# Kernel optimization log

Measured on AMD Instinct MI355X. Metric: run time of the kernel, lower is better.

## Reference

```python
import jax, jax.numpy as jnp
import numpy as np

VOCAB = 32000; PAD = 0
NHID = 512; H = 8; NK = 64; NV = 64; NL = 4
B = 16; S = 511; L = S + 1
N = B * S            # graph nodes after reshape(-1, n_hid)
E = 131072           # edges per graph
EPS = 1e-5
PATTERN = [0, 0, 1, 1, 0, 0, 1, 1]  # n_head==8 -> [gt,gt,attr,attr,gt,gt,attr,attr]


def setup_inputs() -> dict:
    key = jax.random.key(0)
    ks = iter(jax.random.split(key, 48))
    r = lambda *sh: jax.random.normal(next(ks), sh, jnp.float32) * 0.02
    inp = {}
    emb = jax.random.normal(next(ks), (VOCAB, NHID), jnp.float32) * 0.1
    inp['in_embed_w'] = emb.at[PAD].set(0.0)            # padding_idx row is zero
    inp['pos_embed_w'] = jax.random.normal(next(ks), (L, NHID), jnp.float32) * 0.1
    inp['qkv_w'] = r(NL, NHID, H * (2 * NK + NV)); inp['qkv_b'] = r(NL, H * (2 * NK + NV))
    inp['attn_out_w'] = r(NL, H * NV, NHID); inp['attn_out_b'] = r(NL, NHID)
    inp['ff1_w'] = r(NL, NHID, 4 * NHID); inp['ff1_b'] = r(NL, 4 * NHID)
    inp['ff2_w'] = r(NL, 4 * NHID, NHID); inp['ff2_b'] = r(NL, NHID)
    inp['sage1_w'] = r(H, NHID, NHID); inp['sage1_b'] = r(H, NHID)
    inp['sage2_w'] = r(H, NHID, NHID); inp['sage2_b'] = r(H, NHID)
    inp['gc3_w'] = r(H, NHID, NHID // H); inp['gc3_b'] = r(H, NHID // H)
    inp['gcn_ff1_w'] = r(NHID, NHID); inp['gcn_ff1_b'] = r(NHID)
    inp['gcn_ff2_w'] = r(NHID, NHID); inp['gcn_ff2_b'] = r(NHID)
    inp['ln_g'] = jnp.ones((NHID,), jnp.float32)
    inp['ln_b'] = jnp.zeros((NHID,), jnp.float32)
    inp['in_idxs'] = jax.random.randint(next(ks), (B, S), 1, VOCAB)
    inp['mask'] = jnp.ones((B, L, H, L), dtype=bool)
    inp['gt_src'] = jax.random.randint(next(ks), (E,), 0, N)
    inp['gt_dst'] = jax.random.randint(next(ks), (E,), 0, N)
    inp['attr_src'] = jax.random.randint(next(ks), (E,), 0, N)
    inp['attr_dst'] = jax.random.randint(next(ks), (E,), 0, N)
    return inp


def _ln(x, g, b):
    mu = x.mean(-1, keepdims=True)
    v = ((x - mu) ** 2).mean(-1, keepdims=True)
    return (x - mu) / jnp.sqrt(v + EPS) * g + b


def _encode(in_embed_w, pos_embed_w, qkv_w, qkv_b, attn_out_w, attn_out_b,
            ff1_w, ff1_b, ff2_w, ff2_b, sage1_w, sage1_b, sage2_w, sage2_b,
            gc3_w, gc3_b, gcn_ff1_w, gcn_ff1_b, gcn_ff2_w, gcn_ff2_b, ln_g, ln_b,
            in_idxs, mask, gt_src, gt_dst, attr_src, attr_dst):
    # --- embed (pad one pad-token column at the front) ---
    pad_idxs = jnp.pad(in_idxs, ((0, 0), (1, 0)), constant_values=PAD)
    h = in_embed_w[pad_idxs] + pos_embed_w[jnp.arange(L)]        # [B,L,NHID]
    m = mask.transpose(0, 2, 1, 3)                               # [B,H,L,L]
    # --- transformer blocks ---
    for l in range(NL):
        qkv = (h @ qkv_w[l] + qkv_b[l]).reshape(B, L, H, 2 * NK + NV).transpose(0, 2, 1, 3)
        q, k, v = qkv[..., :NK], qkv[..., NK:2 * NK], qkv[..., 2 * NK:]
        sc = jnp.einsum('bhik,bhjk->bhij', q, k) / np.float32(np.sqrt(NK))
        sc = jnp.where(m, sc, -jnp.inf)
        a = jax.nn.softmax(sc, axis=-1)
        o = jnp.einsum('bhij,bhjd->bhid', a, v).transpose(0, 2, 1, 3).reshape(B, L, H * NV)
        attn_ret = h + (o @ attn_out_w[l] + attn_out_b[l])       # attn module returns x + out
        x = h + attn_ret                                         # block adds x again (faithful)
        h = x + (jax.nn.relu(x @ ff1_w[l] + ff1_b[l]) @ ff2_w[l] + ff2_b[l])
    zg, hg = h[:, 0], h[:, 1:]                                   # [B,NHID], [B,S,NHID]
    # --- GCN over flattened nodes ---
    xf = hg.reshape(N, NHID)
    def deg(idx):
        return jax.ops.segment_sum(jnp.ones((E,), jnp.float32), idx, num_segments=N)
    gdata = []
    for src, dst in ((gt_src, gt_dst), (attr_src, attr_dst)):
        gdata.append((src, dst, deg(dst), deg(src)))             # (src, dst, in_deg, out_deg)
    outs = []
    for i in range(H):
        src, dst, ind, outd = gdata[PATTERN[i]]
        def sage(x, W, b):
            # DGL SAGEConv 'gcn': (sum_neigh + self) / (in_deg + 1) then linear
            agg = jax.ops.segment_sum(x[src], dst, num_segments=N)
            return ((agg + x) / (ind + 1.0)[:, None]) @ W + b
        o = sage(xf, sage1_w[i], sage1_b[i])
        o = sage(o, sage2_w[i], sage2_b[i])
        # DGL GraphConv norm='both' (in>out so weight first)
        f = (o @ gc3_w[i]) * (jnp.maximum(outd, 1.0) ** -0.5)[:, None]
        agg = jax.ops.segment_sum(f[src], dst, num_segments=N)
        outs.append(agg * (jnp.maximum(ind, 1.0) ** -0.5)[:, None] + gc3_b[i])
    xc = jnp.concatenate(outs, axis=-1).reshape(B, S, NHID)
    x = hg + _ln(xc, ln_g, ln_b)
    ff = jax.nn.relu(x @ gcn_ff1_w + gcn_ff1_b) @ gcn_ff2_w + gcn_ff2_b
    zbar = x + _ln(ff, ln_g, ln_b)
    return zbar, zg


def reference(in_embed_w, pos_embed_w, qkv_w, qkv_b, attn_out_w, attn_out_b,
              ff1_w, ff1_b, ff2_w, ff2_b, sage1_w, sage1_b, sage2_w, sage2_b,
              gc3_w, gc3_b, gcn_ff1_w, gcn_ff1_b, gcn_ff2_w, gcn_ff2_b, ln_g, ln_b,
              in_idxs, mask, gt_src, gt_dst, attr_src, attr_dst):
    return _encode(in_embed_w, pos_embed_w, qkv_w, qkv_b, attn_out_w, attn_out_b,
                   ff1_w, ff1_b, ff2_w, ff2_b, sage1_w, sage1_b, sage2_w, sage2_b,
                   gc3_w, gc3_b, gcn_ff1_w, gcn_ff1_b, gcn_ff2_w, gcn_ff2_b, ln_g, ln_b,
                   in_idxs, mask, gt_src, gt_dst, attr_src, attr_dst)
```

## Files before the change

### kernel.cpp

```cpp
#include <hip/hip_runtime.h>
#include <hip/hip_bf16.h>

typedef __hip_bfloat16 bf16;
typedef unsigned short u16;
typedef __attribute__((ext_vector_type(8))) short s16x8;
typedef __attribute__((ext_vector_type(4))) float f32x4;

__device__ __forceinline__ float bfb(unsigned short b) {
    union { unsigned u; float f; } v; v.u = ((unsigned)b) << 16; return v.f;
}
__device__ __forceinline__ float ldin(const void* p, size_t i, bool f32) {
    return f32 ? ((const float*)p)[i] : bfb(((const unsigned short*)p)[i]);
}
__device__ __forceinline__ void ld4(const void* p, size_t i, bool f32,
                                    float& x, float& y, float& z, float& w) {
    if (f32) {
        float4 v = *reinterpret_cast<const float4*>((const float*)p + i);
        x = v.x; y = v.y; z = v.z; w = v.w;
    } else {
        ushort4 u = *reinterpret_cast<const ushort4*>((const unsigned short*)p + i);
        x = bfb(u.x); y = bfb(u.y); z = bfb(u.z); w = bfb(u.w);
    }
}
__device__ __forceinline__ u16 f2b(float x) {
    bf16 h = __float2bfloat16(x);
    return *reinterpret_cast<u16*>(&h);
}
__device__ __forceinline__ void split2(float x, u16& h, u16& l) {
    unsigned u = __float_as_uint(x);
    h = (u16)(u >> 16);
    float rem = x - __uint_as_float(u & 0xFFFF0000u);
    l = f2b(rem);
}

constexpr int C_B = 16, C_S = 511, C_L = 512, C_NHID = 512;
constexpr int C_N = C_B * C_S;
constexpr int C_MTOK = C_B * C_L;
constexpr int C_E = 131072;
constexpr int C_QKVD = 1536;

enum : size_t {
    OFF_H     = 0,
    OFF_QKV   = 4194304,
    OFF_O     = 16777216,
    OFF_X     = 20971520,
    OFF_MID   = 25165824,
    OFF_PRE   = 41943040,
    OFF_T8    = OFF_PRE,
    OFF_GCAT0 = OFF_PRE + 262144,
    OFF_GCAT1 = OFF_GCAT0 + 131072,
    OFF_DCAT0 = OFF_GCAT1 + 131072,
    OFF_DCAT1 = OFF_DCAT0 + 256,
    OFF_DEG   = OFF_DCAT1 + 256,
    OFF_FLAG  = OFF_DEG + 32768
};

__global__ void detect_kernel(const unsigned* __restrict__ g, int* __restrict__ flag) {
    *flag = (g[0] == 0x3F800000u) ? 1 : 0;
}

__global__ __launch_bounds__(256) void embed_kernel(
    const void* __restrict__ emb, const void* __restrict__ pos,
    const int* __restrict__ idxs, const int* __restrict__ flag,
    float* __restrict__ h)
{
    const bool f = (*flag) != 0;
    int token = blockIdx.x;
    int tid = threadIdx.x;
    int b = token >> 9, t = token & 511;
    int id = (t == 0) ? 0 : idxs[b * C_S + t - 1];
    size_t eo = (size_t)id * C_NHID, po = (size_t)t * C_NHID, ho = (size_t)token * C_NHID;
    h[ho + tid]       = ldin(emb, eo + tid, f)       + ldin(pos, po + tid, f);
    h[ho + tid + 256] = ldin(emb, eo + tid + 256, f) + ldin(pos, po + tid + 256, f);
}

__global__ __launch_bounds__(256) void wtrans2_kernel(
    const void* __restrict__ Wsrc, size_t srcOff, const int* __restrict__ flag,
    u16* __restrict__ Bh, u16* __restrict__ Bl, int K, int N)
{
    const bool f = (*flag) != 0;
    __shared__ float s[32][33];
    int nb = blockIdx.x << 5, kb = blockIdx.y << 5;
    int c = threadIdx.x & 31, r0 = (threadIdx.x >> 5) << 2;
#pragma unroll
    for (int i = 0; i < 4; ++i)
        s[r0 + i][c] = ldin(Wsrc, srcOff + (size_t)(kb + r0 + i) * N + nb + c, f);
    __syncthreads();
#pragma unroll
    for (int i = 0; i < 4; ++i) {
        u16 h, l;
        split2(s[c][r0 + i], h, l);
        size_t o = (size_t)(nb + r0 + i) * K + kb + c;
        Bh[o] = h; Bl[o] = l;
    }
}

__global__ __launch_bounds__(256, 2) void msgemm_kernel(
    const float* __restrict__ A,
    const u16* __restrict__ Bh, const u16* __restrict__ Bl,
    const void* __restrict__ biasB, size_t bOff,
    const float* __restrict__ biasF,
    const float* __restrict__ res, float resScale,
    const float* __restrict__ rowDeg, int relu,
    const int* __restrict__ flag,
    float* __restrict__ C, int M, int K, int Nc, int ldc)
{
    const bool f32in = (*flag) != 0;
    __shared__ __align__(16) u16 sAh[128][40];
    __shared__ __align__(16) u16 sAl[128][40];
    __shared__ __align__(16) u16 sBh[64][40];
    __shared__ __align__(16) u16 sBl[64][40];
    const int tid = threadIdx.x;
    const int bm = blockIdx.y << 7, bn = blockIdx.x << 6;
    const int lane = tid & 63, lr = lane & 15, lg = lane >> 4;
    const int wave = tid >> 6, wm = wave >> 1, wn = wave & 1;

    f32x4 acc[4][2];
#pragma unroll
    for (int m = 0; m < 4; ++m)
#pragma unroll
        for (int n = 0; n < 2; ++n) {
            f32x4 z = {0.f, 0.f, 0.f, 0.f};
            acc[m][n] = z;
        }

    const int sr = tid >> 1, sk = (tid & 1) << 4;
    const int am = bm + sr;
    const bool aok = am < M;
    const float* ap = A + (size_t)am * K + sk;
    const int brn = tid >> 2, bk = (tid & 3) << 3;
    const u16* bph = Bh + (size_t)(bn + brn) * K + bk;
    const u16* bpl = Bl + (size_t)(bn + brn) * K + bk;

    for (int k0 = 0; k0 < K; k0 += 32) {
        u16 tah[16], tal[16];
        if (aok) {
#pragma unroll
            for (int i = 0; i < 16; i += 4) {
                float4 v = *reinterpret_cast<const float4*>(ap + k0 + i);
                split2(v.x, tah[i],     tal[i]);
                split2(v.y, tah[i + 1], tal[i + 1]);
                split2(v.z, tah[i + 2], tal[i + 2]);
                split2(v.w, tah[i + 3], tal[i + 3]);
            }
        } else {
#pragma unroll
            for (int i = 0; i < 16; ++i) { tah[i] = 0; tal[i] = 0; }
        }
        s16x8 bh0 = *reinterpret_cast<const s16x8*>(bph + k0);
        s16x8 bl0 = *reinterpret_cast<const s16x8*>(bpl + k0);

        *reinterpret_cast<s16x8*>(&sAh[sr][sk])     = *reinterpret_cast<s16x8*>(&tah[0]);
        *reinterpret_cast<s16x8*>(&sAh[sr][sk + 8]) = *reinterpret_cast<s16x8*>(&tah[8]);
        *reinterpret_cast<s16x8*>(&sAl[sr][sk])     = *reinterpret_cast<s16x8*>(&tal[0]);
        *reinterpret_cast<s16x8*>(&sAl[sr][sk + 8]) = *reinterpret_cast<s16x8*>(&tal[8]);
        *reinterpret_cast<s16x8*>(&sBh[brn][bk]) = bh0;
        *reinterpret_cast<s16x8*>(&sBl[brn][bk]) = bl0;
        __syncthreads();

        s16x8 fah[4], fal[4], fbh[2], fbl[2];
#pragma unroll
        for (int m = 0; m < 4; ++m) {
            fah[m] = *reinterpret_cast<const s16x8*>(&sAh[wm * 64 + m * 16 + lr][lg * 8]);
            fal[m] = *reinterpret_cast<const s16x8*>(&sAl[wm * 64 + m * 16 + lr][lg * 8]);
        }
#pragma unroll
        for (int n = 0; n < 2; ++n) {
            fbh[n] = *reinterpret_cast<const s16x8*>(&sBh[wn * 32 + n * 16 + lr][lg * 8]);
            fbl[n] = *reinterpret_cast<const s16x8*>(&sBl[wn * 32 + n * 16 + lr][lg * 8]);
        }
#pragma unroll
        for (int m = 0; m < 4; ++m)
#pragma unroll
            for (int n = 0; n < 2; ++n) {
                acc[m][n] = __builtin_amdgcn_mfma_f32_16x16x32_bf16(fah[m], fbh[n], acc[m][n], 0, 0, 0);
                acc[m][n] = __builtin_amdgcn_mfma_f32_16x16x32_bf16(fah[m], fbl[n], acc[m][n], 0, 0, 0);
                acc[m][n] = __builtin_amdgcn_mfma_f32_16x16x32_bf16(fal[m], fbh[n], acc[m][n], 0, 0, 0);
            }
        __syncthreads();
    }

#pragma unroll
    for (int m = 0; m < 4; ++m) {
#pragma unroll
        for (int r = 0; r < 4; ++r) {
            int row = bm + wm * 64 + m * 16 + lg * 4 + r;
            if (row >= M) continue;
            float rs = rowDeg ? rsqrtf(fmaxf(rowDeg[row], 1.f)) : 1.f;
#pragma unroll
            for (int n = 0; n < 2; ++n) {
                int col = bn + wn * 32 + n * 16 + lr;
                float v = acc[m][n][r];
                if (biasB) v += ldin(biasB, bOff + col, f32in);
                if (biasF) v += biasF[col];
                v *= rs;
                if (res) v += resScale * res[(size_t)row * Nc + col];
                if (relu) v = fmaxf(v, 0.f);
                C[(size_t)row * ldc + col] = v;
            }
        }
    }
}

__global__ __launch_bounds__(256) void mattn_kernel(
    const float* __restrict__ qkv, float* __restrict__ o_out)
{
    __shared__ __align__(16) u16 sKh[64][72], sKl[64][72];
    __shared__ __align__(16) u16 sVh[64][72], sVl[64][72];
    __shared__ __align__(16) u16 sPh[4][16][72], sPl[4][16][72];
    const int blk = blockIdx.x;
    const int b = blk >> 6, h = (blk >> 3) & 7, qt = blk & 7;
    const int tid = threadIdx.x;
    const int lane = tid & 63, lr = lane & 15, lg = lane >> 4;
    const int w = tid >> 6;

    s16x8 qh[2], ql[2];
    {
        const float* qp = qkv + (size_t)(b * C_L + qt * 64 + w * 16 + lr) * C_QKVD + h * 192;
#pragma unroll
        for (int c = 0; c < 2; ++c) {
            int d0 = c * 32 + lg * 8;
            u16 th[8], tl[8];
#pragma unroll
            for (int i = 0; i < 8; i += 4) {
                float4 v = *reinterpret_cast<const float4*>(qp + d0 + i);
                split2(v.x * 0.125f, th[i],     tl[i]);
                split2(v.y * 0.125f, th[i + 1], tl[i + 1]);
                split2(v.z * 0.125f, th[i + 2], tl[i + 2]);
                split2(v.w * 0.125f, th[i + 3], tl[i + 3]);
            }
            qh[c] = *reinterpret_cast<s16x8*>(th);
            ql[c] = *reinterpret_cast<s16x8*>(tl);
        }
    }

    f32x4 accO[4];
#pragma unroll
    for (int n = 0; n < 4; ++n) { f32x4 z = {0.f, 0.f, 0.f, 0.f}; accO[n] = z; }
    float m[4] = {-3.0e38f, -3.0e38f, -3.0e38f, -3.0e38f};
    float l[4] = {0.f, 0.f, 0.f, 0.f};

    const float* kvb = qkv + (size_t)b * C_L * C_QKVD + h * 192;
    const int kp = tid >> 2;
    const int d0 = (tid & 3) << 4;

    for (int jt = 0; jt < 8; ++jt) {
        __syncthreads();
        {
            const float* kr = kvb + (size_t)(jt * 64 + kp) * C_QKVD + 64 + d0;
            const float* vr = kr + 64;
#pragma unroll
            for (int i = 0; i < 16; i += 4) {
                float4 kv = *reinterpret_cast<const float4*>(kr + i);
                float4 vv = *reinterpret_cast<const float4*>(vr + i);
                u16 th[4], tl[4];
                split2(kv.x, th[0], tl[0]); split2(kv.y, th[1], tl[1]);
                split2(kv.z, th[2], tl[2]); split2(kv.w, th[3], tl[3]);
                *reinterpret_cast<ushort4*>(&sKh[kp][d0 + i]) = *reinterpret_cast<ushort4*>(th);
                *reinterpret_cast<ushort4*>(&sKl[kp][d0 + i]) = *reinterpret_cast<ushort4*>(tl);
                u16 hh, ll;
                split2(vv.x, hh, ll); sVh[d0 + i][kp]     = hh; sVl[d0 + i][kp]     = ll;
                split2(vv.y, hh, ll); sVh[d0 + i + 1][kp] = hh; sVl[d0 + i + 1][kp] = ll;
                split2(vv.z, hh, ll); sVh[d0 + i + 2][kp] = hh; sVl[d0 + i + 2][kp] = ll;
                split2(vv.w, hh, ll); sVh[d0 + i + 3][kp] = hh; sVl[d0 + i + 3][kp] = ll;
            }
        }
        __syncthreads();

        f32x4 accS[4];
#pragma unroll
        for (int n = 0; n < 4; ++n) { f32x4 z = {0.f, 0.f, 0.f, 0.f}; accS[n] = z; }
#pragma unroll
        for (int n = 0; n < 4; ++n)
#pragma unroll
            for (int c = 0; c < 2; ++c) {
                s16x8 kh = *reinterpret_cast<const s16x8*>(&sKh[n * 16 + lr][c * 32 + lg * 8]);
                s16x8 kl = *reinterpret_cast<const s16x8*>(&sKl[n * 16 + lr][c * 32 + lg * 8]);
                accS[n] = __builtin_amdgcn_mfma_f32_16x16x32_bf16(qh[c], kh, accS[n], 0, 0, 0);
                accS[n] = __builtin_amdgcn_mfma_f32_16x16x32_bf16(qh[c], kl, accS[n], 0, 0, 0);
                accS[n] = __builtin_amdgcn_mfma_f32_16x16x32_bf16(ql[c], kh, accS[n], 0, 0, 0);
            }

#pragma unroll
        for (int r = 0; r < 4; ++r) {
            float mt = fmaxf(fmaxf(accS[0][r], accS[1][r]), fmaxf(accS[2][r], accS[3][r]));
            mt = fmaxf(mt, __shfl_xor(mt, 1));
            mt = fmaxf(mt, __shfl_xor(mt, 2));
            mt = fmaxf(mt, __shfl_xor(mt, 4));
            mt = fmaxf(mt, __shfl_xor(mt, 8));
            float mn = fmaxf(m[r], mt);
            float corr = __expf(m[r] - mn);
            m[r] = mn;
            float ps = 0.f;
#pragma unroll
            for (int n = 0; n < 4; ++n) {
                float p = __expf(accS[n][r] - mn);
                accS[n][r] = p;
                ps += p;
            }
            ps += __shfl_xor(ps, 1);
            ps += __shfl_xor(ps, 2);
            ps += __shfl_xor(ps, 4);
            ps += __shfl_xor(ps, 8);
            l[r] = l[r] * corr + ps;
#pragma unroll
            for (int n2 = 0; n2 < 4; ++n2) accO[n2][r] *= corr;
        }

#pragma unroll
        for (int r = 0; r < 4; ++r)
#pragma unroll
            for (int n = 0; n < 4; ++n) {
                u16 hh, ll;
                split2(accS[n][r], hh, ll);
                sPh[w][lg * 4 + r][n * 16 + lr] = hh;
                sPl[w][lg * 4 + r][n * 16 + lr] = ll;
            }
        __syncthreads();

#pragma unroll
        for (int n2 = 0; n2 < 4; ++n2)
#pragma unroll
            for (int c = 0; c < 2; ++c) {
                s16x8 ph = *reinterpret_cast<const s16x8*>(&sPh[w][lr][c * 32 + lg * 8]);
                s16x8 pl = *reinterpret_cast<const s16x8*>(&sPl[w][lr][c * 32 + lg * 8]);
                s16x8 vh = *reinterpret_cast<const s16x8*>(&sVh[n2 * 16 + lr][c * 32 + lg * 8]);
                s16x8 vl = *reinterpret_cast<const s16x8*>(&sVl[n2 * 16 + lr][c * 32 + lg * 8]);
                accO[n2] = __builtin_amdgcn_mfma_f32_16x16x32_bf16(ph, vh, accO[n2], 0, 0, 0);
                accO[n2] = __builtin_amdgcn_mfma_f32_16x16x32_bf16(ph, vl, accO[n2], 0, 0, 0);
                accO[n2] = __builtin_amdgcn_mfma_f32_16x16x32_bf16(pl, vh, accO[n2], 0, 0, 0);
            }
    }

#pragma unroll
    for (int r = 0; r < 4; ++r) {
        float inv = 1.f / l[r];
        float* op = o_out + (size_t)(b * C_L + qt * 64 + w * 16 + lg * 4 + r) * C_NHID + h * 64;
#pragma unroll
        for (int n2 = 0; n2 < 4; ++n2)
            op[n2 * 16 + lr] = accO[n2][r] * inv;
    }
}

__global__ __launch_bounds__(256) void sgemm64b_kernel(
    const void* __restrict__ A, int aIn, size_t aOff, size_t zA,
    const void* __restrict__ Wt, int wIn, size_t wOff, size_t zW,
    const int* __restrict__ flag,
    float* __restrict__ C, size_t zC, int M, int K, int Nc)
{
    const bool f32in = (*flag) != 0;
    const bool aF32 = aIn ? f32in : true;
    const bool wF32 = wIn ? f32in : true;
    const size_t za = aOff + (size_t)blockIdx.z * zA;
    const size_t zw = wOff + (size_t)blockIdx.z * zW;
    float* Cz = C + (size_t)blockIdx.z * zC;

    __shared__ float sA[16][68];
    __shared__ float sB[16][68];
    const int tid = threadIdx.x;
    const int tx = tid & 15, ty = tid >> 4;
    const int bm = blockIdx.y << 6, bn = blockIdx.x << 6;
    float acc[4][4] = {};
    const int la_r = tid >> 2;
    const int la_c = (tid & 3) << 2;
    const int lb_r = tid >> 4;
    const int lb_c = (tid & 15) << 2;

    for (int k0 = 0; k0 < K; k0 += 16) {
        float a0, a1, a2, a3, b0, b1, b2, b3;
        ld4(A, za + (size_t)(bm + la_r) * K + k0 + la_c, aF32, a0, a1, a2, a3);
        ld4(Wt, zw + (size_t)(k0 + lb_r) * Nc + bn + lb_c, wF32, b0, b1, b2, b3);
        sA[la_c + 0][la_r] = a0; sA[la_c + 1][la_r] = a1;
        sA[la_c + 2][la_r] = a2; sA[la_c + 3][la_r] = a3;
        sB[lb_r][lb_c + 0] = b0; sB[lb_r][lb_c + 1] = b1;
        sB[lb_r][lb_c + 2] = b2; sB[lb_r][lb_c + 3] = b3;
        __syncthreads();
#pragma unroll
        for (int kk = 0; kk < 16; ++kk) {
            float av[4], bv[4];
#pragma unroll
            for (int i = 0; i < 4; ++i) av[i] = sA[kk][(ty << 2) + i];
#pragma unroll
            for (int j = 0; j < 4; ++j) bv[j] = sB[kk][(tx << 2) + j];
#pragma unroll
            for (int i = 0; i < 4; ++i)
#pragma unroll
                for (int j = 0; j < 4; ++j)
                    acc[i][j] += av[i] * bv[j];
        }
        __syncthreads();
    }
#pragma unroll
    for (int i = 0; i < 4; ++i)
#pragma unroll
        for (int j = 0; j < 4; ++j)
            Cz[(size_t)(bm + (ty << 2) + i) * Nc + bn + (tx << 2) + j] = acc[i][j];
}

__global__ __launch_bounds__(256) void gcatT2_kernel(
    const float* __restrict__ Gtmp,
    u16* __restrict__ G0h, u16* __restrict__ G0l,
    u16* __restrict__ G1h, u16* __restrict__ G1l)
{
    int idx = blockIdx.x * 256 + threadIdx.x;
    int i = idx >> 15, rem = idx & 32767;
    int k = rem >> 6, c = rem & 63;
    int g = (i >> 1) & 1;
    int slot = (i & 1) + ((i >> 2) << 1);
    u16 h, l;
    split2(Gtmp[idx], h, l);
    size_t o = (size_t)(slot * 64 + c) * 512 + k;
    if (g) { G1h[o] = h; G1l[o] = l; }
    else   { G0h[o] = h; G0l[o] = l; }
}

__global__ __launch_bounds__(256) void xfcopy_kernel(
    const float* __restrict__ h, float* __restrict__ xf)
{
    int idx = blockIdx.x * 256 + threadIdx.x;
    int n = idx >> 9, c = idx & 511;
    int b = n / C_S;
    int s = n - b * C_S;
    xf[idx] = h[(((size_t)(b * C_L + 1 + s)) << 9) + c];
}

__global__ __launch_bounds__(256) void degi_kernel(
    const int* __restrict__ gs, const int* __restrict__ gd,
    const int* __restrict__ as_, const int* __restrict__ ad,
    int* __restrict__ ideg0, int* __restrict__ ideg1,
    float* __restrict__ outd0, float* __restrict__ outd1)
{
    int e = blockIdx.x * 256 + threadIdx.x;
    if (e >= C_E) return;
    atomicAdd(&ideg0[gd[e]], 1);
    atomicAdd(&ideg1[ad[e]], 1);
    atomicAdd(&outd0[gs[e]], 1.f);
    atomicAdd(&outd1[as_[e]], 1.f);
}

__global__ __launch_bounds__(1024) void scan_kernel(
    const int* __restrict__ i0, const int* __restrict__ i1,
    int* __restrict__ r0, int* __restrict__ r1)
{
    __shared__ int part[1024];
    const int t = threadIdx.x;
    const int* d = blockIdx.x ? i1 : i0;
    int* rs = blockIdx.x ? r1 : r0;
    int v[8]; int s = 0;
#pragma unroll
    for (int i = 0; i < 8; ++i) {
        int idx = t * 8 + i;
        v[i] = (idx < C_N) ? d[idx] : 0;
        s += v[i];
    }
    part[t] = s;
    __syncthreads();
    for (int off = 1; off < 1024; off <<= 1) {
        int x = (t >= off) ? part[t - off] : 0;
        __syncthreads();
        part[t] += x;
        __syncthreads();
    }
    int run = part[t] - s;
#pragma unroll
    for (int i = 0; i < 8; ++i) {
        int idx = t * 8 + i;
        if (idx <= C_N) rs[idx] = run;
        run += v[i];
    }
}

__global__ __launch_bounds__(256) void fill_kernel(
    const int* __restrict__ gs, const int* __restrict__ gd,
    const int* __restrict__ as_, const int* __restrict__ ad,
    const int* __restrict__ rs0, const int* __restrict__ rs1,
    int* __restrict__ cur0, int* __restrict__ cur1,
    int* __restrict__ csr0, int* __restrict__ csr1)
{
    int e = blockIdx.x * 256 + threadIdx.x;
    if (e >= C_E) return;
    int d0 = gd[e];
    int p = atomicAdd(&cur0[d0], 1);
    csr0[rs0[d0] + p] = gs[e];
    int d1 = ad[e];
    int q = atomicAdd(&cur1[d1], 1);
    csr1[rs1[d1] + q] = as_[e];
}

__global__ __launch_bounds__(256) void gatherA_kernel(
    const float* __restrict__ X, const int* __restrict__ csr,
    const int* __restrict__ rs, float* __restrict__ Y)
{
    const int n = blockIdx.x;
    const int tid = threadIdx.x;
    const int s0 = rs[n], s1 = rs[n + 1];
    const size_t o = (size_t)n * 512;
    float a0 = X[o + tid], a1 = X[o + tid + 256];
    for (int e = s0; e < s1; ++e) {
        const size_t so = (size_t)csr[e] * 512;
        a0 += X[so + tid];
        a1 += X[so + tid + 256];
    }
    const float r = 1.f / (float)(s1 - s0 + 1);
    Y[o + tid] = a0 * r;
    Y[o + tid + 256] = a1 * r;
}

__global__ __launch_bounds__(256) void gatherF_kernel(
    const float* __restrict__ F, const int* __restrict__ csr,
    const int* __restrict__ rs, float* __restrict__ xcagg,
    int c0, int c1, int c2, int c3)
{
    const int n = blockIdx.x;
    const int c = threadIdx.x;
    const int s0 = rs[n], s1 = rs[n + 1];
    float acc = 0.f;
    for (int e = s0; e < s1; ++e)
        acc += F[(size_t)csr[e] * 256 + c];
    const int s = c >> 6, cc = c & 63;
    const int cmap = (s == 0) ? c0 : (s == 1) ? c1 : (s == 2) ? c2 : c3;
    xcagg[(size_t)n * 512 + cmap + cc] = acc;
}

__global__ __launch_bounds__(256) void fxc_kernel(
    float* __restrict__ xcagg, const int* __restrict__ rs0,
    const int* __restrict__ rs1, const void* __restrict__ g3b,
    const int* __restrict__ flag)
{
    const bool f = (*flag) != 0;
    unsigned idx = blockIdx.x * 256 + threadIdx.x;
    int n = idx >> 7;
    int c = (idx & 127) << 2;
    int hh = c >> 6;
    int g = (hh >> 1) & 1;
    const int* rs = g ? rs1 : rs0;
    float ind = (float)(rs[n + 1] - rs[n]);
    float r = rsqrtf(fmaxf(ind, 1.f));
    size_t o = (size_t)n * 512 + c;
    float4 v = *reinterpret_cast<float4*>(xcagg + o);
    v.x = v.x * r + ldin(g3b, c, f);     v.y = v.y * r + ldin(g3b, c + 1, f);
    v.z = v.z * r + ldin(g3b, c + 2, f); v.w = v.w * r + ldin(g3b, c + 3, f);
    *reinterpret_cast<float4*>(xcagg + o) = v;
}

__global__ __launch_bounds__(64) void dvec_kernel(
    const void* __restrict__ s1b, const void* __restrict__ s2b,
    const void* __restrict__ g3w, const float* __restrict__ T8,
    const int* __restrict__ flag, float* __restrict__ dc0, float* __restrict__ dc1)
{
    const bool f = (*flag) != 0;
    int i = blockIdx.x, c = threadIdx.x;
    const float* T = T8 + (size_t)i * 512 * 64;
    float acc = 0.f;
    for (int k = 0; k < 512; ++k)
        acc += ldin(s1b, (size_t)i * 512 + k, f) * T[k * 64 + c]
             + ldin(s2b, (size_t)i * 512 + k, f) * ldin(g3w, (size_t)i * 32768 + (size_t)k * 64 + c, f);
    int g = (i >> 1) & 1;
    int slot = (i & 1) + ((i >> 2) << 1);
    (g ? dc1 : dc0)[slot * 64 + c] = acc;
}

__global__ __launch_bounds__(256) void ln_kernel(
    const float* __restrict__ in, const float* __restrict__ res,
    const void* __restrict__ gw, const void* __restrict__ bw,
    const int* __restrict__ flag, float* __restrict__ out)
{
    const bool f = (*flag) != 0;
    int row = blockIdx.x;
    int tid = threadIdx.x;
    const float* x = in + (size_t)row * 512;
    float v0 = x[tid], v1 = x[tid + 256];
    __shared__ float red[4];
    float s = v0 + v1;
#pragma unroll
    for (int off = 32; off > 0; off >>= 1) s += __shfl_down(s, off);
    if ((tid & 63) == 0) red[tid >> 6] = s;
    __syncthreads();
    float mu = (red[0] + red[1] + red[2] + red[3]) * (1.f / 512.f);
    __syncthreads();
    float d0 = v0 - mu, d1 = v1 - mu;
    s = d0 * d0 + d1 * d1;
#pragma unroll
    for (int off = 32; off > 0; off >>= 1) s += __shfl_down(s, off);
    if ((tid & 63) == 0) red[tid >> 6] = s;
    __syncthreads();
    float var = (red[0] + red[1] + red[2] + red[3]) * (1.f / 512.f);
    float rstd = rsqrtf(var + 1e-5f);
    size_t o = (size_t)row * 512;
    float r0 = d0 * rstd * ldin(gw, tid, f)       + ldin(bw, tid, f);
    float r1 = d1 * rstd * ldin(gw, tid + 256, f) + ldin(bw, tid + 256, f);
    if (res) { r0 += res[o + tid]; r1 += res[o + tid + 256]; }
    out[o + tid] = r0;
    out[o + tid + 256] = r1;
}

__global__ __launch_bounds__(256) void out_zbar_kernel(
    const float* __restrict__ z, void* __restrict__ out, const int* __restrict__ flag)
{
    const bool f = (*flag) != 0;
    int idx = blockIdx.x * 256 + threadIdx.x;
    if (f) ((float*)out)[idx] = z[idx];
    else   ((bf16*)out)[idx]  = __float2bfloat16(z[idx]);
}

__global__ __launch_bounds__(256) void out_zg_kernel(
    const float* __restrict__ h, void* __restrict__ out, const int* __restrict__ flag)
{
    const bool f = (*flag) != 0;
    int idx = blockIdx.x * 256 + threadIdx.x;
    int b = idx >> 9, c = idx & 511;
    float v = h[(size_t)b * C_L * 512 + c];
    size_t o = (size_t)C_N * 512 + idx;
    if (f) ((float*)out)[o] = v;
    else   ((bf16*)out)[o]  = __float2bfloat16(v);
}

static inline void msgemm(hipStream_t st,
    const float* A, const u16* Bh, const u16* Bl,
    const void* biasB, size_t bOff, const float* biasF,
    const float* res, float resScale, const float* rowDeg, int relu,
    const int* flag, float* C, int M, int K, int Nc, int ldc)
{
    dim3 g(Nc / 64, (M + 127) / 128);
    msgemm_kernel<<<g, dim3(256), 0, st>>>(A, Bh, Bl, biasB, bOff, biasF,
                                           res, resScale, rowDeg, relu, flag,
                                           C, M, K, Nc, ldc);
}

static inline void wtrans2(hipStream_t st, const void* Wsrc, size_t srcOff,
                           const int* flag, u16* Bh, u16* Bl, int K, int N)
{
    wtrans2_kernel<<<dim3(N / 32, K / 32), dim3(256), 0, st>>>(
        Wsrc, srcOff, flag, Bh, Bl, K, N);
}

extern "C" void kernel_launch(void* const* d_in, const int* in_sizes, int n_in,
                              void* d_out, int out_size, void* d_ws, size_t ws_size,
                              hipStream_t stream)
{
    const void* emb   = d_in[0];
    const void* pos   = d_in[1];
    const void* qkv_w = d_in[2];
    const void* qkv_b = d_in[3];
    const void* aow   = d_in[4];
    const void* aob   = d_in[5];
    const void* ff1w  = d_in[6];
    const void* ff1b  = d_in[7];
    const void* ff2w  = d_in[8];
    const void* ff2b  = d_in[9];
    const void* s1w   = d_in[10];
    const void* s1b   = d_in[11];
    const void* s2w   = d_in[12];
    const void* s2b   = d_in[13];
    const void* g3w   = d_in[14];
    const void* g3b   = d_in[15];
    const void* gf1w  = d_in[16];
    const void* gf1b  = d_in[17];
    const void* gf2w  = d_in[18];
    const void* gf2b  = d_in[19];
    const void* lng   = d_in[20];
    const void* lnb   = d_in[21];
    const int* idxs   = (const int*)d_in[22];
    const int* gts    = (const int*)d_in[24];
    const int* gtd    = (const int*)d_in[25];
    const int* ats    = (const int*)d_in[26];
    const int* atd    = (const int*)d_in[27];

    float* W = (float*)d_ws;
    float* h    = W + OFF_H;
    float* qkvb = W + OFF_QKV;
    float* ob   = W + OFF_O;
    float* xb   = W + OFF_X;
    float* midb = W + OFF_MID;
    int* flag   = (int*)(W + OFF_FLAG);

    detect_kernel<<<dim3(1), dim3(1), 0, stream>>>((const unsigned*)lng, flag);

    embed_kernel<<<dim3(C_MTOK), dim3(256), 0, stream>>>(emb, pos, idxs, flag, h);

    u16* qkvT = (u16*)ob;
    u16* aoT  = (u16*)midb;
    u16* ffT  = (u16*)qkvb;

    for (int l = 0; l < 4; ++l) {
        wtrans2(stream, qkv_w, (size_t)l * 512 * 1536, flag,
                qkvT, qkvT + 786432, 512, 1536);
        msgemm(stream, h, qkvT, qkvT + 786432, qkv_b, (size_t)l * 1536, nullptr,
               nullptr, 0.f, nullptr, 0, flag, qkvb, C_MTOK, 512, 1536, 1536);
        mattn_kernel<<<dim3(1024), dim3(256), 0, stream>>>(qkvb, ob);
        wtrans2(stream, aow, (size_t)l * 512 * 512, flag,
                aoT, aoT + 262144, 512, 512);
        msgemm(stream, ob, aoT, aoT + 262144, aob, (size_t)l * 512, nullptr,
               h, 2.f, nullptr, 0, flag, xb, C_MTOK, 512, 512, 512);
        wtrans2(stream, ff1w, (size_t)l * 512 * 2048, flag,
                ffT, ffT + 1048576, 512, 2048);
        msgemm(stream, xb, ffT, ffT + 1048576, ff1b, (size_t)l * 2048, nullptr,
               nullptr, 0.f, nullptr, 1, flag, midb, C_MTOK, 512, 2048, 2048);
        wtrans2(stream, ff2w, (size_t)l * 2048 * 512, flag,
                ffT + 2097152, ffT + 3145728, 2048, 512);
        msgemm(stream, midb, ffT + 2097152, ffT + 3145728, ff2b, (size_t)l * 512, nullptr,
               xb, 1.f, nullptr, 0, flag, h, C_MTOK, 2048, 512, 512);
    }

    float* xf    = ob;
    float* Z0    = qkvb;
    float* Z1    = qkvb + 4194304;
    float* Yb    = qkvb + 8388608;
    float* Gtmp  = Yb;
    float* Fb    = xb;
    float* zbar  = xb;
    float* xcagg = midb;
    float* xgnn  = midb + 4194304;
    float* fmid  = midb + 8388608;
    float* fout  = midb + 12582912;
    float* T8    = W + OFF_T8;
    float* dc0   = W + OFF_DCAT0;
    float* dc1   = W + OFF_DCAT1;
    float* outd0 = W + OFF_DEG;
    float* outd1 = outd0 + 8192;
    u16* GcT0h = (u16*)(W + OFF_GCAT0);
    u16* GcT0l = GcT0h + 131072;
    u16* GcT1h = (u16*)(W + OFF_GCAT1);
    u16* GcT1l = GcT1h + 131072;
    u16* gfT   = (u16*)Yb;

    int* ibase = (int*)fmid;
    int* rs0   = ibase;
    int* rs1   = ibase + 8208;
    int* ideg0 = ibase + 16416;
    int* ideg1 = ibase + 24608;
    int* cur0  = ibase + 32800;
    int* cur1  = ibase + 40992;
    int* csr0  = ibase + 49184;
    int* csr1  = ibase + 180256;

    xfcopy_kernel<<<dim3(C_N * 512 / 256), dim3(256), 0, stream>>>(h, xf);

    (void)hipMemsetAsync(ideg0, 0, 2 * 8192 * sizeof(int), stream);
    (void)hipMemsetAsync(cur0, 0, 2 * 8192 * sizeof(int), stream);
    (void)hipMemsetAsync(outd0, 0, 2 * 8192 * sizeof(float), stream);
    degi_kernel<<<dim3(C_E / 256), dim3(256), 0, stream>>>(
        gts, gtd, ats, atd, ideg0, ideg1, outd0, outd1);
    scan_kernel<<<dim3(2), dim3(1024), 0, stream>>>(ideg0, ideg1, rs0, rs1);
    fill_kernel<<<dim3(C_E / 256), dim3(256), 0, stream>>>(
        gts, gtd, ats, atd, rs0, rs1, cur0, cur1, csr0, csr1);

    sgemm64b_kernel<<<dim3(1, 8, 8), dim3(256), 0, stream>>>(
        s2w, 1, 0, 262144, g3w, 1, 0, 32768, flag, T8, 32768, 512, 512, 64);
    sgemm64b_kernel<<<dim3(1, 8, 8), dim3(256), 0, stream>>>(
        s1w, 1, 0, 262144, T8, 0, 0, 32768, flag, Gtmp, 32768, 512, 512, 64);
    gcatT2_kernel<<<dim3(1024), dim3(256), 0, stream>>>(Gtmp, GcT0h, GcT0l, GcT1h, GcT1l);
    dvec_kernel<<<dim3(8), dim3(64), 0, stream>>>(s1b, s2b, g3w, T8, flag, dc0, dc1);

    gatherA_kernel<<<dim3(C_N), dim3(256), 0, stream>>>(xf, csr0, rs0, Yb);
    gatherA_kernel<<<dim3(C_N), dim3(256), 0, stream>>>(Yb, csr0, rs0, Z0);
    gatherA_kernel<<<dim3(C_N), dim3(256), 0, stream>>>(xf, csr1, rs1, Yb);
    gatherA_kernel<<<dim3(C_N), dim3(256), 0, stream>>>(Yb, csr1, rs1, Z1);

    msgemm(stream, Z0, GcT0h, GcT0l, nullptr, 0, dc0, nullptr, 0.f, outd0, 0, flag,
           Fb, C_N, 512, 256, 256);
    gatherF_kernel<<<dim3(C_N), dim3(256), 0, stream>>>(
        Fb, csr0, rs0, xcagg, 0, 64, 256, 320);
    msgemm(stream, Z1, GcT1h, GcT1l, nullptr, 0, dc1, nullptr, 0.f, outd1, 0, flag,
           Fb, C_N, 512, 256, 256);
    gatherF_kernel<<<dim3(C_N), dim3(256), 0, stream>>>(
        Fb, csr1, rs1, xcagg, 128, 192, 384, 448);
    fxc_kernel<<<dim3(C_N * 128 / 256), dim3(256), 0, stream>>>(
        xcagg, rs0, rs1, g3b, flag);

    ln_kernel<<<dim3(C_N), dim3(256), 0, stream>>>(xcagg, xf, lng, lnb, flag, xgnn);
    wtrans2(stream, gf1w, 0, flag, gfT, gfT + 262144, 512, 512);
    msgemm(stream, xgnn, gfT, gfT + 262144, gf1b, 0, nullptr,
           nullptr, 0.f, nullptr, 1, flag, fmid, C_N, 512, 512, 512);
    wtrans2(stream, gf2w, 0, flag, gfT + 524288, gfT + 786432, 512, 512);
    msgemm(stream, fmid, gfT + 524288, gfT + 786432, gf2b, 0, nullptr,
           nullptr, 0.f, nullptr, 0, flag, fout, C_N, 512, 512, 512);
    ln_kernel<<<dim3(C_N), dim3(256), 0, stream>>>(fout, xgnn, lng, lnb, flag, zbar);

    out_zbar_kernel<<<dim3(C_N * 512 / 256), dim3(256), 0, stream>>>(zbar, d_out, flag);
    out_zg_kernel<<<dim3(32), dim3(256), 0, stream>>>(h, d_out, flag);
}
```

Measured before the change: 2.462 ms.

## Add 128x128-tile split-bf16 GEMM for QKV/FF1 and parallelize dvec reduction

Adds a new MFMA GEMM kernel that uses 128x128 output tiles, with each wave computing a 64x64 sub-tile. It is used for the wide QKV and FF1 projections so each loaded A/B tile is reused more, cutting shared and global memory traffic per FLOP. Separately, the dvec kernel now splits its K loop across 8 wavefronts and combines the partial sums in shared memory. The larger tile raises register pressure (64 accumulator floats per lane), which may limit occupancy.

```diff
diff --git a/kernel.cpp b/kernel.cpp
--- a/kernel.cpp
+++ b/kernel.cpp
@@ -202,6 +202,109 @@
     }
 }
 
+__global__ __launch_bounds__(256, 2) void msgemm2_kernel(
+    const float* __restrict__ A,
+    const u16* __restrict__ Bh, const u16* __restrict__ Bl,
+    const void* __restrict__ biasB, size_t bOff,
+    const int relu, const int* __restrict__ flag,
+    float* __restrict__ C, int M, int K, int Nc, int ldc)
+{
+    const bool f32in = (*flag) != 0;
+    __shared__ __align__(16) u16 sAh[128][40];
+    __shared__ __align__(16) u16 sAl[128][40];
+    __shared__ __align__(16) u16 sBh[128][40];
+    __shared__ __align__(16) u16 sBl[128][40];
+    const int tid = threadIdx.x;
+    const int bm = blockIdx.y << 7, bn = blockIdx.x << 7;
+    const int lane = tid & 63, lr = lane & 15, lg = lane >> 4;
+    const int wave = tid >> 6, wm = wave >> 1, wn = wave & 1;
+
+    f32x4 acc[4][4];
+#pragma unroll
+    for (int m = 0; m < 4; ++m)
+#pragma unroll
+        for (int n = 0; n < 4; ++n) {
+            f32x4 z = {0.f, 0.f, 0.f, 0.f};
+            acc[m][n] = z;
+        }
+
+    const int sr = tid >> 1, sk = (tid & 1) << 4;
+    const int am = bm + sr;
+    const bool aok = am < M;
+    const float* ap = A + (size_t)am * K + sk;
+    const u16* bph = Bh + (size_t)(bn + sr) * K + sk;
+    const u16* bpl = Bl + (size_t)(bn + sr) * K + sk;
+
+    for (int k0 = 0; k0 < K; k0 += 32) {
+        u16 tah[16], tal[16];
+        if (aok) {
+#pragma unroll
+            for (int i = 0; i < 16; i += 4) {
+                float4 v = *reinterpret_cast<const float4*>(ap + k0 + i);
+                split2(v.x, tah[i],     tal[i]);
+                split2(v.y, tah[i + 1], tal[i + 1]);
+                split2(v.z, tah[i + 2], tal[i + 2]);
+                split2(v.w, tah[i + 3], tal[i + 3]);
+            }
+        } else {
+#pragma unroll
+            for (int i = 0; i < 16; ++i) { tah[i] = 0; tal[i] = 0; }
+        }
+        s16x8 bh0 = *reinterpret_cast<const s16x8*>(bph + k0);
+        s16x8 bh1 = *reinterpret_cast<const s16x8*>(bph + k0 + 8);
+        s16x8 bl0 = *reinterpret_cast<const s16x8*>(bpl + k0);
+        s16x8 bl1 = *reinterpret_cast<const s16x8*>(bpl + k0 + 8);
+
+        *reinterpret_cast<s16x8*>(&sAh[sr][sk])     = *reinterpret_cast<s16x8*>(&tah[0]);
+        *reinterpret_cast<s16x8*>(&sAh[sr][sk + 8]) = *reinterpret_cast<s16x8*>(&tah[8]);
+        *reinterpret_cast<s16x8*>(&sAl[sr][sk])     = *reinterpret_cast<s16x8*>(&tal[0]);
+        *reinterpret_cast<s16x8*>(&sAl[sr][sk + 8]) = *reinterpret_cast<s16x8*>(&tal[8]);
+        *reinterpret_cast<s16x8*>(&sBh[sr][sk])     = bh0;
+        *reinterpret_cast<s16x8*>(&sBh[sr][sk + 8]) = bh1;
+        *reinterpret_cast<s16x8*>(&sBl[sr][sk])     = bl0;
+        *reinterpret_cast<s16x8*>(&sBl[sr][sk + 8]) = bl1;
+        __syncthreads();
+
+        s16x8 fah[4], fal[4], fbh[4], fbl[4];
+#pragma unroll
+        for (int m = 0; m < 4; ++m) {
+            fah[m] = *reinterpret_cast<const s16x8*>(&sAh[wm * 64 + m * 16 + lr][lg * 8]);
+            fal[m] = *reinterpret_cast<const s16x8*>(&sAl[wm * 64 + m * 16 + lr][lg * 8]);
+        }
+#pragma unroll
+        for (int n = 0; n < 4; ++n) {
+            fbh[n] = *reinterpret_cast<const s16x8*>(&sBh[wn * 64 + n * 16 + lr][lg * 8]);
+            fbl[n] = *reinterpret_cast<const s16x8*>(&sBl[wn * 64 + n * 16 + lr][lg * 8]);
+        }
+#pragma unroll
+        for (int m = 0; m < 4; ++m)
+#pragma unroll
+            for (int n = 0; n < 4; ++n) {
+                acc[m][n] = __builtin_amdgcn_mfma_f32_16x16x32_bf16(fah[m], fbh[n], acc[m][n], 0, 0, 0);
+                acc[m][n] = __builtin_amdgcn_mfma_f32_16x16x32_bf16(fah[m], fbl[n], acc[m][n], 0, 0, 0);
+                acc[m][n] = __builtin_amdgcn_mfma_f32_16x16x32_bf16(fal[m], fbh[n], acc[m][n], 0, 0, 0);
+            }
+        __syncthreads();
+    }
+
+#pragma unroll
+    for (int m = 0; m < 4; ++m) {
+#pragma unroll
+        for (int r = 0; r < 4; ++r) {
+            int row = bm + wm * 64 + m * 16 + lg * 4 + r;
+            if (row >= M) continue;
+#pragma unroll
+            for (int n = 0; n < 4; ++n) {
+                int col = bn + wn * 64 + n * 16 + lr;
+                float v = acc[m][n][r];
+                if (biasB) v += ldin(biasB, bOff + col, f32in);
+                if (relu) v = fmaxf(v, 0.f);
+                C[(size_t)row * ldc + col] = v;
+            }
+        }
+    }
+}
+
 __global__ __launch_bounds__(256) void mattn_kernel(
     const float* __restrict__ qkv, float* __restrict__ o_out)
 {
@@ -543,21 +646,31 @@
     *reinterpret_cast<float4*>(xcagg + o) = v;
 }
 
-__global__ __launch_bounds__(64) void dvec_kernel(
+__global__ __launch_bounds__(512) void dvec_kernel(
     const void* __restrict__ s1b, const void* __restrict__ s2b,
     const void* __restrict__ g3w, const float* __restrict__ T8,
     const int* __restrict__ flag, float* __restrict__ dc0, float* __restrict__ dc1)
 {
     const bool f = (*flag) != 0;
-    int i = blockIdx.x, c = threadIdx.x;
-    const float* T = T8 + (size_t)i * 512 * 64;
+    const int i = blockIdx.x;
+    const int c = threadIdx.x & 63;
+    const int kg = threadIdx.x >> 6;
+    const float* T = T8 + (size_t)i * 32768;
     float acc = 0.f;
-    for (int k = 0; k < 512; ++k)
+    const int kbeg = kg * 64, kend = kbeg + 64;
+    for (int k = kbeg; k < kend; ++k)
         acc += ldin(s1b, (size_t)i * 512 + k, f) * T[k * 64 + c]
              + ldin(s2b, (size_t)i * 512 + k, f) * ldin(g3w, (size_t)i * 32768 + (size_t)k * 64 + c, f);
-    int g = (i >> 1) & 1;
-    int slot = (i & 1) + ((i >> 2) << 1);
-    (g ? dc1 : dc0)[slot * 64 + c] = acc;
+    __shared__ float red[8][64];
+    red[kg][c] = acc;
+    __syncthreads();
+    if (kg == 0) {
+        float v = red[0][c] + red[1][c] + red[2][c] + red[3][c]
+                + red[4][c] + red[5][c] + red[6][c] + red[7][c];
+        int g = (i >> 1) & 1;
+        int slot = (i & 1) + ((i >> 2) << 1);
+        (g ? dc1 : dc0)[slot * 64 + c] = v;
+    }
 }
 
 __global__ __launch_bounds__(256) void ln_kernel(
@@ -625,6 +738,16 @@
     msgemm_kernel<<<g, dim3(256), 0, st>>>(A, Bh, Bl, biasB, bOff, biasF,
                                            res, resScale, rowDeg, relu, flag,
                                            C, M, K, Nc, ldc);
+}
+
+static inline void msgemm2(hipStream_t st,
+    const float* A, const u16* Bh, const u16* Bl,
+    const void* biasB, size_t bOff, int relu,
+    const int* flag, float* C, int M, int K, int Nc, int ldc)
+{
+    dim3 g(Nc / 128, (M + 127) / 128);
+    msgemm2_kernel<<<g, dim3(256), 0, st>>>(A, Bh, Bl, biasB, bOff, relu, flag,
+                                            C, M, K, Nc, ldc);
 }
 
 static inline void wtrans2(hipStream_t st, const void* Wsrc, size_t srcOff,
@@ -685,8 +808,8 @@
     for (int l = 0; l < 4; ++l) {
         wtrans2(stream, qkv_w, (size_t)l * 512 * 1536, flag,
                 qkvT, qkvT + 786432, 512, 1536);
-        msgemm(stream, h, qkvT, qkvT + 786432, qkv_b, (size_t)l * 1536, nullptr,
-               nullptr, 0.f, nullptr, 0, flag, qkvb, C_MTOK, 512, 1536, 1536);
+        msgemm2(stream, h, qkvT, qkvT + 786432, qkv_b, (size_t)l * 1536,
+                0, flag, qkvb, C_MTOK, 512, 1536, 1536);
         mattn_kernel<<<dim3(1024), dim3(256), 0, stream>>>(qkvb, ob);
         wtrans2(stream, aow, (size_t)l * 512 * 512, flag,
                 aoT, aoT + 262144, 512, 512);
@@ -694,8 +817,8 @@
                h, 2.f, nullptr, 0, flag, xb, C_MTOK, 512, 512, 512);
         wtrans2(stream, ff1w, (size_t)l * 512 * 2048, flag,
                 ffT, ffT + 1048576, 512, 2048);
-        msgemm(stream, xb, ffT, ffT + 1048576, ff1b, (size_t)l * 2048, nullptr,
-               nullptr, 0.f, nullptr, 1, flag, midb, C_MTOK, 512, 2048, 2048);
+        msgemm2(stream, xb, ffT, ffT + 1048576, ff1b, (size_t)l * 2048,
+                1, flag, midb, C_MTOK, 512, 2048, 2048);
         wtrans2(stream, ff2w, (size_t)l * 2048 * 512, flag,
                 ffT + 2097152, ffT + 3145728, 2048, 512);
         msgemm(stream, midb, ffT + 2097152, ffT + 3145728, ff2b, (size_t)l * 512, nullptr,
@@ -750,7 +873,7 @@
     sgemm64b_kernel<<<dim3(1, 8, 8), dim3(256), 0, stream>>>(
         s1w, 1, 0, 262144, T8, 0, 0, 32768, flag, Gtmp, 32768, 512, 512, 64);
     gcatT2_kernel<<<dim3(1024), dim3(256), 0, stream>>>(Gtmp, GcT0h, GcT0l, GcT1h, GcT1l);
-    dvec_kernel<<<dim3(8), dim3(64), 0, stream>>>(s1b, s2b, g3w, T8, flag, dc0, dc1);
+    dvec_kernel<<<dim3(8), dim3(512), 0, stream>>>(s1b, s2b, g3w, T8, flag, dc0, dc1);
 
     gatherA_kernel<<<dim3(C_N), dim3(256), 0, stream>>>(xf, csr0, rs0, Yb);
     gatherA_kernel<<<dim3(C_N), dim3(256), 0, stream>>>(Yb, csr0, rs0, Z0);
```

Result: faster. 2.246 ms (-8.8%).
